# Optimization experiments

Hardware: AMD Instinct MI355X
Metric: run time of the kernel (lower is better)

Reference implementation:

```python
import jax, jax.numpy as jnp
import numpy as np

H = 64        # gru_hiddens
HEADS = 4     # n_heads
HID = 64      # n_hidden (is_concat=False -> out_features)
RT = 4        # role_types
APT = 3       # agents per type
N_AMB = 1023  # ambiguous agents; N = 1 + N_AMB = 1024
SLOPE = 0.2


def _leaky(x):
    return jnp.where(x >= 0, x, SLOPE * x)


def _linear(x, W, b):
    return x @ W.T + b


def setup_inputs() -> dict:
    key = jax.random.key(0)
    ks = jax.random.split(key, 18)
    s = 0.1
    return {
        "hidden": jax.random.normal(ks[0], (1, H), jnp.float32),
        "ambiguous": jax.random.normal(ks[1], (N_AMB, H), jnp.float32),
        "type_agents": jax.random.normal(ks[2], (RT, APT, 1, H), jnp.float32),
        # per-role-type routing MLPs and merge/self MLPs
        "W_self": jax.random.normal(ks[3], (H, H), jnp.float32) * s,
        "b_self": jnp.zeros((H,), jnp.float32),
        "W_merge": jax.random.normal(ks[4], (H, 2 * H), jnp.float32) * s,
        "b_merge": jnp.zeros((H,), jnp.float32),
        "W_trans": jax.random.normal(ks[5], (RT, H, H), jnp.float32) * s,
        "b_trans": jnp.zeros((RT, H), jnp.float32),
        # GATv2 params (no biases)
        "W_l": jax.random.normal(ks[6], (HEADS * HID, H), jnp.float32) * s,
        "W_r": jax.random.normal(ks[7], (HEADS * HID, H), jnp.float32) * s,
        "w_attn": jax.random.normal(ks[8], (HID,), jnp.float32) * s,
        # type_define MLP: 2H -> 64 -> 128 -> RT
        "Wd0": jax.random.normal(ks[9], (64, 2 * H), jnp.float32) * s,
        "bd0": jnp.zeros((64,), jnp.float32),
        "Wd1": jax.random.normal(ks[10], (128, 64), jnp.float32) * s,
        "bd1": jnp.zeros((128,), jnp.float32),
        "Wd2": jax.random.normal(ks[11], (RT, 128), jnp.float32) * s,
        "bd2": jnp.zeros((RT,), jnp.float32),
    }


def reference(hidden, ambiguous, type_agents,
              W_self, b_self, W_merge, b_merge, W_trans, b_trans,
              W_l, W_r, w_attn,
              Wd0, bd0, Wd1, bd1, Wd2, bd2):
    # per-role-type routing + merge
    hidden_1 = _linear(hidden, W_self, b_self)  # [1, H]
    for t in range(RT):
        # mean over agents of trans_mlp[t](agent)
        tmp = (jnp.einsum('aih,oh->aio', type_agents[t], W_trans[t]) + b_trans[t]).mean(axis=0)
        hidden_1 = _leaky(_linear(jnp.concatenate([hidden_1, tmp], axis=-1), W_merge, b_merge))

    h = jnp.concatenate([hidden_1, ambiguous], axis=0)  # [N, H], N = 1 + N_AMB
    n = h.shape[0]

    # GATv2 dense pairwise attention (adjacency all-True; dropout in eval = identity)
    g_l = (h @ W_l.T).reshape(n, HEADS, HID)
    g_r = (h @ W_r.T).reshape(n, HEADS, HID)
    # g_sum[i, j] = g_l[j] + g_r[i]  -> [N, N, HEADS, HID]
    g_sum = g_l[None, :, :, :] + g_r[:, None, :, :]
    e = jnp.einsum('ijhf,f->ijh', _leaky(g_sum), w_attn)  # [N, N, HEADS]
    a = jax.nn.softmax(e, axis=1)
    attn_res = jnp.einsum('ijh,jhf->ihf', a, g_r)  # [N, HEADS, HID]
    gat_out = attn_res.mean(axis=1)  # is_concat=False -> mean over heads, [N, HID]

    hidden_2 = gat_out[0]  # [HID]
    rep = jnp.broadcast_to(hidden_2[None, :], (ambiguous.shape[0], HID))
    x = jnp.concatenate([ambiguous, rep], axis=-1)  # [N_AMB, 2H]
    x = _leaky(_linear(x, Wd0, bd0))
    x = _leaky(_linear(x, Wd1, bd1))
    x = _linear(x, Wd2, bd2)
    return jax.nn.sigmoid(x)  # [N_AMB, RT]
```

## Files before the change

### kernel.cpp

```cpp
#include <hip/hip_runtime.h>
#include <math.h>

#define SLOPE 0.2f

__device__ __forceinline__ float leaky(float x) { return x >= 0.f ? x : SLOPE * x; }


__global__ __launch_bounds__(256) void kA_gat(
    const float* __restrict__ hidden, const float* __restrict__ ambiguous,
    const float* __restrict__ type_agents,
    const float* __restrict__ W_self, const float* __restrict__ b_self,
    const float* __restrict__ W_merge, const float* __restrict__ b_merge,
    const float* __restrict__ W_trans, const float* __restrict__ b_trans,
    const float* __restrict__ W_l, const float* __restrict__ W_r,
    const float* __restrict__ w_attn, float* __restrict__ ws)
{
    __shared__ __align__(16) float sh[128];
    __shared__ __align__(16) float tm[64];
    __shared__ __align__(16) float h1[64];
    __shared__ __align__(16) float hrow[4][64];
    const int t = threadIdx.x;
    const int o = t & 63;
    const bool lead = (t < 64);

    float hv = 0.f;
    if (lead) {
        float acc = b_self[o];
        const float4* w4 = (const float4*)(W_self + o * 64);
#pragma unroll
        for (int k = 0; k < 16; k++) {
            float4 w = w4[k];
            acc += w.x * hidden[k*4+0] + w.y * hidden[k*4+1]
                 + w.z * hidden[k*4+2] + w.w * hidden[k*4+3];
        }
        hv = acc;
    }
    for (int tt = 0; tt < 4; tt++) {
        if (lead) {
            sh[o] = hv;
            tm[o] = (type_agents[tt*192 + o] + type_agents[tt*192 + 64 + o]
                   + type_agents[tt*192 + 128 + o]) * (1.f / 3.f);
        }
        __syncthreads();
        if (lead) {
            float tv = b_trans[tt*64 + o];
            const float4* w4 = (const float4*)(W_trans + tt*4096 + o*64);
#pragma unroll
            for (int k = 0; k < 16; k++) {
                float4 w = w4[k];
                tv += w.x * tm[k*4+0] + w.y * tm[k*4+1]
                    + w.z * tm[k*4+2] + w.w * tm[k*4+3];
            }
            sh[64 + o] = tv;
        }
        __syncthreads();
        if (lead) {
            float acc = b_merge[o];
            const float4* w4 = (const float4*)(W_merge + o * 128);
#pragma unroll
            for (int k = 0; k < 32; k++) {
                float4 w = w4[k];
                acc += w.x * sh[k*4+0] + w.y * sh[k*4+1]
                     + w.z * sh[k*4+2] + w.w * sh[k*4+3];
            }
            hv = leaky(acc);
        }
        __syncthreads();
    }
    if (lead) h1[o] = hv;

    float4 wl[16], wr[16];
    {
        const float4* Wl4 = (const float4*)(W_l + t * 64);
        const float4* Wr4 = (const float4*)(W_r + t * 64);
#pragma unroll
        for (int k = 0; k < 16; k++) { wl[k] = Wl4[k]; wr[k] = Wr4[k]; }
    }
    __syncthreads();

    float g0 = 0.f;
#pragma unroll
    for (int k = 0; k < 16; k++) {
        float4 w = wr[k];
        g0 += w.x * h1[k*4+0] + w.y * h1[k*4+1] + w.z * h1[k*4+2] + w.w * h1[k*4+3];
    }

    {
        int r = t >> 6;
        int j = blockIdx.x * 4 + r;
        hrow[r][o] = (j == 0) ? h1[o] : ambiguous[(j - 1) * 64 + o];
    }
    __syncthreads();

    float accl[4] = {0.f, 0.f, 0.f, 0.f};
    float accr[4] = {0.f, 0.f, 0.f, 0.f};
#pragma unroll
    for (int kk = 0; kk < 16; kk++) {
        float4 a = wl[kk], b = wr[kk];
#pragma unroll
        for (int r = 0; r < 4; r++) {
            float x0 = hrow[r][kk*4+0], x1 = hrow[r][kk*4+1];
            float x2 = hrow[r][kk*4+2], x3 = hrow[r][kk*4+3];
            accl[r] += a.x*x0 + a.y*x1 + a.z*x2 + a.w*x3;
            accr[r] += b.x*x0 + b.y*x1 + b.z*x2 + b.w*x3;
        }
    }

    const int head = t >> 6;
    const float wa = w_attn[o];
    float numsum = 0.f, denp = 0.f;
#pragma unroll
    for (int r = 0; r < 4; r++) {
        float ec = leaky(accl[r] + g0) * wa;
#pragma unroll
        for (int off = 32; off; off >>= 1) ec += __shfl_xor(ec, off, 64);
        float w = expf(ec);
        numsum += w * accr[r];
        denp   += w;
    }
    atomicAdd(&ws[t], numsum);
    if (o == 0) atomicAdd(&ws[256 + head], denp);
}

__global__ __launch_bounds__(256) void kB_mlp(
    const float* __restrict__ ambiguous,
    const float* __restrict__ Wd0, const float* __restrict__ bd0,
    const float* __restrict__ Wd1, const float* __restrict__ bd1,
    const float* __restrict__ Wd2, const float* __restrict__ bd2,
    const float* __restrict__ ws, float* __restrict__ out)
{
    __shared__ __align__(16) float x[4][128];
    __shared__ __align__(16) float y0[4][64];
    __shared__ __align__(16) float y1[4][128];
    const int t  = threadIdx.x;
    const int r0 = blockIdx.x * 4;
    const int r  = t >> 6, k = t & 63;

    {
        int row = r0 + r;
        x[r][k] = (row < 1023) ? ambiguous[row * 64 + k] : 0.f;
    }
    if (t < 64) {
        float s = 0.f;
#pragma unroll
        for (int h = 0; h < 4; h++) s += ws[h*64 + t] / ws[256 + h];
        float h2 = 0.25f * s;
        x[0][64 + t] = h2; x[1][64 + t] = h2; x[2][64 + t] = h2; x[3][64 + t] = h2;
    }
    __syncthreads();

    {
        float acc = bd0[k];
        const float4* w4 = (const float4*)(Wd0 + k * 128);
        const float4* xr = (const float4*)(&x[r][0]);
#pragma unroll
        for (int kk = 0; kk < 32; kk++) {
            float4 w = w4[kk]; float4 xv = xr[kk];
            acc += w.x*xv.x + w.y*xv.y + w.z*xv.z + w.w*xv.w;
        }
        y0[r][k] = leaky(acc);
    }
    __syncthreads();

#pragma unroll
    for (int rep = 0; rep < 2; rep++) {
        int idx = rep * 256 + t;
        int rr = idx >> 7, oo = idx & 127;
        float acc = bd1[oo];
        const float4* w4 = (const float4*)(Wd1 + oo * 64);
        const float4* yr = (const float4*)(&y0[rr][0]);
#pragma unroll
        for (int kk = 0; kk < 16; kk++) {
            float4 w = w4[kk]; float4 yv = yr[kk];
            acc += w.x*yv.x + w.y*yv.y + w.z*yv.z + w.w*yv.w;
        }
        y1[rr][oo] = leaky(acc);
    }
    __syncthreads();

    if (t < 16) {
        int rr = t >> 2, c = t & 3;
        int row = r0 + rr;
        if (row < 1023) {
            float acc = bd2[c];
            const float4* w4 = (const float4*)(Wd2 + c * 128);
            const float4* yr = (const float4*)(&y1[rr][0]);
#pragma unroll
            for (int kk = 0; kk < 32; kk++) {
                float4 w = w4[kk]; float4 yv = yr[kk];
                acc += w.x*yv.x + w.y*yv.y + w.z*yv.z + w.w*yv.w;
            }
            out[row * 4 + c] = 1.f / (1.f + expf(-acc));
        }
    }
}

extern "C" void kernel_launch(void* const* d_in, const int* in_sizes, int n_in,
                              void* d_out, int out_size, void* d_ws, size_t ws_size,
                              hipStream_t stream)
{
    const float* hidden      = (const float*)d_in[0];
    const float* ambiguous   = (const float*)d_in[1];
    const float* type_agents = (const float*)d_in[2];
    const float* W_self      = (const float*)d_in[3];
    const float* b_self      = (const float*)d_in[4];
    const float* W_merge     = (const float*)d_in[5];
    const float* b_merge     = (const float*)d_in[6];
    const float* W_trans     = (const float*)d_in[7];
    const float* b_trans     = (const float*)d_in[8];
    const float* W_l         = (const float*)d_in[9];
    const float* W_r         = (const float*)d_in[10];
    const float* w_attn      = (const float*)d_in[11];
    const float* Wd0         = (const float*)d_in[12];
    const float* bd0         = (const float*)d_in[13];
    const float* Wd1         = (const float*)d_in[14];
    const float* bd1         = (const float*)d_in[15];
    const float* Wd2         = (const float*)d_in[16];
    const float* bd2         = (const float*)d_in[17];
    float* ws  = (float*)d_ws;
    float* out = (float*)d_out;

    kA_gat<<<256, 256, 0, stream>>>(hidden, ambiguous, type_agents,
                                    W_self, b_self, W_merge, b_merge,
                                    W_trans, b_trans, W_l, W_r, w_attn, ws);
    kB_mlp<<<256, 256, 0, stream>>>(ambiguous, Wd0, bd0, Wd1, bd1, Wd2, bd2, ws, out);
}
```

Before: 126.2 us.

## Replace GAT atomics with per-block partials, halve blocks, overlap row loads with prologue

The attention kernel now runs 128 blocks of 8 rows each instead of 256 blocks of 4. Each block writes its partial numerator and denominator to its own workspace slot instead of issuing global atomicAdds, and the MLP kernel reduces the 128 partials itself. Only wave 0 computes the serial routing/merge prologue, using intra-wave fences instead of block barriers, while the other waves preload ambiguous rows concurrently. The aim is to remove atomic contention and the serial barrier chain, at the cost of every MLP block redundantly summing 128 partials and higher register pressure from 8-row accumulators.

```diff
diff --git a/kernel.cpp b/kernel.cpp
--- a/kernel.cpp
+++ b/kernel.cpp
@@ -2,6 +2,9 @@
 #include <math.h>
 
 #define SLOPE 0.2f
+#define KA_BLK 128
+#define KA_ROWS 8
+#define PART_STRIDE 320
 
 __device__ __forceinline__ float leaky(float x) { return x >= 0.f ? x : SLOPE * x; }
 
@@ -18,43 +21,61 @@
     __shared__ __align__(16) float sh[128];
     __shared__ __align__(16) float tm[64];
     __shared__ __align__(16) float h1[64];
-    __shared__ __align__(16) float hrow[4][64];
+    __shared__ __align__(16) float hrow[KA_ROWS][64];
+
     const int t = threadIdx.x;
     const int o = t & 63;
-    const bool lead = (t < 64);
-
-    float hv = 0.f;
-    if (lead) {
-        float acc = b_self[o];
-        const float4* w4 = (const float4*)(W_self + o * 64);
-#pragma unroll
-        for (int k = 0; k < 16; k++) {
-            float4 w = w4[k];
-            acc += w.x * hidden[k*4+0] + w.y * hidden[k*4+1]
-                 + w.z * hidden[k*4+2] + w.w * hidden[k*4+3];
-        }
-        hv = acc;
-    }
-    for (int tt = 0; tt < 4; tt++) {
-        if (lead) {
+    const int r = t >> 6;
+    const int b = blockIdx.x;
+
+    float4 wr[16];
+    {
+        const float4* Wr4 = (const float4*)(W_r + t * 64);
+#pragma unroll
+        for (int k = 0; k < 16; k++) wr[k] = Wr4[k];
+    }
+
+    if (r != 0) {
+        int u = t - 64;
+#pragma unroll
+        for (int i = 0; i < 3; i++) {
+            int idx = u + 192 * i;
+            if (idx < KA_ROWS * 64) {
+                int rl = idx >> 6, c = idx & 63;
+                int j = b * KA_ROWS + rl;
+                hrow[rl][c] = (j == 0) ? 0.f : ambiguous[(j - 1) * 64 + c];
+            }
+        }
+    } else {
+        float hv;
+        {
+            float acc = b_self[o];
+            const float4* w4 = (const float4*)(W_self + o * 64);
+#pragma unroll
+            for (int k = 0; k < 16; k++) {
+                float4 w = w4[k];
+                acc += w.x * hidden[k*4+0] + w.y * hidden[k*4+1]
+                     + w.z * hidden[k*4+2] + w.w * hidden[k*4+3];
+            }
+            hv = acc;
+        }
+        for (int tt = 0; tt < 4; tt++) {
             sh[o] = hv;
             tm[o] = (type_agents[tt*192 + o] + type_agents[tt*192 + 64 + o]
                    + type_agents[tt*192 + 128 + o]) * (1.f / 3.f);
-        }
-        __syncthreads();
-        if (lead) {
+            __threadfence_block();
             float tv = b_trans[tt*64 + o];
-            const float4* w4 = (const float4*)(W_trans + tt*4096 + o*64);
-#pragma unroll
-            for (int k = 0; k < 16; k++) {
-                float4 w = w4[k];
-                tv += w.x * tm[k*4+0] + w.y * tm[k*4+1]
-                    + w.z * tm[k*4+2] + w.w * tm[k*4+3];
+            {
+                const float4* w4 = (const float4*)(W_trans + tt*4096 + o*64);
+#pragma unroll
+                for (int k = 0; k < 16; k++) {
+                    float4 w = w4[k];
+                    tv += w.x * tm[k*4+0] + w.y * tm[k*4+1]
+                        + w.z * tm[k*4+2] + w.w * tm[k*4+3];
+                }
             }
             sh[64 + o] = tv;
-        }
-        __syncthreads();
-        if (lead) {
+            __threadfence_block();
             float acc = b_merge[o];
             const float4* w4 = (const float4*)(W_merge + o * 128);
 #pragma unroll
@@ -64,19 +85,12 @@
                      + w.z * sh[k*4+2] + w.w * sh[k*4+3];
             }
             hv = leaky(acc);
-        }
-        __syncthreads();
-    }
-    if (lead) h1[o] = hv;
-
-    float4 wl[16], wr[16];
-    {
-        const float4* Wl4 = (const float4*)(W_l + t * 64);
-        const float4* Wr4 = (const float4*)(W_r + t * 64);
-#pragma unroll
-        for (int k = 0; k < 16; k++) { wl[k] = Wl4[k]; wr[k] = Wr4[k]; }
-    }
-    __syncthreads();
+            __threadfence_block();
+        }
+        h1[o] = hv;
+    }
+    __syncthreads();
+    if (b == 0 && t < 64) hrow[0][o] = h1[o];
 
     float g0 = 0.f;
 #pragma unroll
@@ -84,42 +98,40 @@
         float4 w = wr[k];
         g0 += w.x * h1[k*4+0] + w.y * h1[k*4+1] + w.z * h1[k*4+2] + w.w * h1[k*4+3];
     }
-
-    {
-        int r = t >> 6;
-        int j = blockIdx.x * 4 + r;
-        hrow[r][o] = (j == 0) ? h1[o] : ambiguous[(j - 1) * 64 + o];
-    }
-    __syncthreads();
-
-    float accl[4] = {0.f, 0.f, 0.f, 0.f};
-    float accr[4] = {0.f, 0.f, 0.f, 0.f};
-#pragma unroll
-    for (int kk = 0; kk < 16; kk++) {
-        float4 a = wl[kk], b = wr[kk];
-#pragma unroll
-        for (int r = 0; r < 4; r++) {
-            float x0 = hrow[r][kk*4+0], x1 = hrow[r][kk*4+1];
-            float x2 = hrow[r][kk*4+2], x3 = hrow[r][kk*4+3];
-            accl[r] += a.x*x0 + a.y*x1 + a.z*x2 + a.w*x3;
-            accr[r] += b.x*x0 + b.y*x1 + b.z*x2 + b.w*x3;
-        }
-    }
-
-    const int head = t >> 6;
+    __syncthreads();
+
+    float accl[KA_ROWS], accr[KA_ROWS];
+#pragma unroll
+    for (int rr = 0; rr < KA_ROWS; rr++) { accl[rr] = 0.f; accr[rr] = 0.f; }
+    {
+        const float4* Wl4 = (const float4*)(W_l + t * 64);
+#pragma unroll
+        for (int kk = 0; kk < 16; kk++) {
+            float4 a = Wl4[kk];
+            float4 c = wr[kk];
+#pragma unroll
+            for (int rr = 0; rr < KA_ROWS; rr++) {
+                float x0 = hrow[rr][kk*4+0], x1 = hrow[rr][kk*4+1];
+                float x2 = hrow[rr][kk*4+2], x3 = hrow[rr][kk*4+3];
+                accl[rr] += a.x*x0 + a.y*x1 + a.z*x2 + a.w*x3;
+                accr[rr] += c.x*x0 + c.y*x1 + c.z*x2 + c.w*x3;
+            }
+        }
+    }
+
     const float wa = w_attn[o];
     float numsum = 0.f, denp = 0.f;
 #pragma unroll
-    for (int r = 0; r < 4; r++) {
-        float ec = leaky(accl[r] + g0) * wa;
+    for (int rr = 0; rr < KA_ROWS; rr++) {
+        float ec = leaky(accl[rr] + g0) * wa;
 #pragma unroll
         for (int off = 32; off; off >>= 1) ec += __shfl_xor(ec, off, 64);
         float w = expf(ec);
-        numsum += w * accr[r];
+        numsum += w * accr[rr];
         denp   += w;
     }
-    atomicAdd(&ws[t], numsum);
-    if (o == 0) atomicAdd(&ws[256 + head], denp);
+    ws[b * PART_STRIDE + t] = numsum;
+    if (o == 0) ws[b * PART_STRIDE + 256 + r] = denp;
 }
 
 __global__ __launch_bounds__(256) void kB_mlp(
@@ -132,33 +144,43 @@
     __shared__ __align__(16) float x[4][128];
     __shared__ __align__(16) float y0[4][64];
     __shared__ __align__(16) float y1[4][128];
+    __shared__ __align__(16) float hs[4][64];
     const int t  = threadIdx.x;
+    const int o  = t & 63;
+    const int r  = t >> 6;
     const int r0 = blockIdx.x * 4;
-    const int r  = t >> 6, k = t & 63;
 
     {
         int row = r0 + r;
-        x[r][k] = (row < 1023) ? ambiguous[row * 64 + k] : 0.f;
-    }
+        x[r][o] = (row < 1023) ? ambiguous[row * 64 + o] : 0.f;
+    }
+
+    float nsum = 0.f;
+#pragma unroll 16
+    for (int bb = 0; bb < KA_BLK; bb++) nsum += ws[bb * PART_STRIDE + t];
+
+    float d = ws[o * PART_STRIDE + 256 + r]
+            + ws[(o + 64) * PART_STRIDE + 256 + r];
+#pragma unroll
+    for (int off = 32; off; off >>= 1) d += __shfl_xor(d, off, 64);
+    hs[r][o] = nsum / d;
+    __syncthreads();
     if (t < 64) {
-        float s = 0.f;
-#pragma unroll
-        for (int h = 0; h < 4; h++) s += ws[h*64 + t] / ws[256 + h];
-        float h2 = 0.25f * s;
-        x[0][64 + t] = h2; x[1][64 + t] = h2; x[2][64 + t] = h2; x[3][64 + t] = h2;
-    }
-    __syncthreads();
-
-    {
-        float acc = bd0[k];
-        const float4* w4 = (const float4*)(Wd0 + k * 128);
+        float h2 = 0.25f * (hs[0][o] + hs[1][o] + hs[2][o] + hs[3][o]);
+        x[0][64 + o] = h2; x[1][64 + o] = h2; x[2][64 + o] = h2; x[3][64 + o] = h2;
+    }
+    __syncthreads();
+
+    {
+        float acc = bd0[o];
+        const float4* w4 = (const float4*)(Wd0 + o * 128);
         const float4* xr = (const float4*)(&x[r][0]);
 #pragma unroll
         for (int kk = 0; kk < 32; kk++) {
             float4 w = w4[kk]; float4 xv = xr[kk];
             acc += w.x*xv.x + w.y*xv.y + w.z*xv.z + w.w*xv.w;
         }
-        y0[r][k] = leaky(acc);
+        y0[r][o] = leaky(acc);
     }
     __syncthreads();
 
@@ -220,8 +242,8 @@
     float* ws  = (float*)d_ws;
     float* out = (float*)d_out;
 
-    kA_gat<<<256, 256, 0, stream>>>(hidden, ambiguous, type_agents,
-                                    W_self, b_self, W_merge, b_merge,
-                                    W_trans, b_trans, W_l, W_r, w_attn, ws);
+    kA_gat<<<KA_BLK, 256, 0, stream>>>(hidden, ambiguous, type_agents,
+                                       W_self, b_self, W_merge, b_merge,
+                                       W_trans, b_trans, W_l, W_r, w_attn, ws);
     kB_mlp<<<256, 256, 0, stream>>>(ambiguous, Wd0, bd0, Wd1, bd1, Wd2, bd2, ws, out);
 }
```

Result: slower. 129.1 us (+2.3%).
